# Kernel tuning notes

Measured on AMD Instinct MI355X. Metric: run time of the kernel, lower is better.

Reference implementation:

```python
import jax, jax.numpy as jnp
import numpy as np

B, S, D, H = 2, 2048, 1024, 16
DH = D // H  # head_dim = 64


def setup_inputs() -> dict:
    key = jax.random.key(0)
    ks = jax.random.split(key, 10)
    inp = {
        "query": jax.random.normal(ks[0], (B, S, D), jnp.float32),
        "key": jax.random.normal(ks[1], (B, S, D), jnp.float32),
        "value": jax.random.normal(ks[2], (B, S, D), jnp.float32),
        "mask": jnp.ones((B, S), jnp.int32),
        # per-head q/k/v projections stacked over the head axis [H, D, DH]
        "Wq": jax.random.normal(ks[3], (H, D, DH), jnp.float32) * 0.02,
        "bq": jnp.zeros((H, DH), jnp.float32),
        "Wk": jax.random.normal(ks[4], (H, D, DH), jnp.float32) * 0.02,
        "bk": jnp.zeros((H, DH), jnp.float32),
        "Wv": jax.random.normal(ks[5], (H, D, DH), jnp.float32) * 0.02,
        "bv": jnp.zeros((H, DH), jnp.float32),
        # output projection fc: Linear(D, D)
        "Wo": jax.random.normal(ks[6], (D, D), jnp.float32) * 0.02,
        "bo": jnp.zeros((D,), jnp.float32),
    }
    return inp


def reference(query, key, value, mask, Wq, bq, Wk, bk, Wv, bv, Wo, bo):
    scale = 1.0 / jnp.sqrt(jnp.asarray(DH, query.dtype))
    # batched per-head projections: [B,S,D] x [H,D,DH] -> [B,H,S,DH]
    q = jnp.einsum('bsd,hde->bhse', query, Wq) + bq[None, :, None, :]
    k = jnp.einsum('bsd,hde->bhse', key, Wk) + bk[None, :, None, :]
    v = jnp.einsum('bsd,hde->bhse', value, Wv) + bv[None, :, None, :]
    # scaled dot-product attention scores [B,H,Sq,Sk]
    scores = jnp.einsum('bhqe,bhke->bhqk', q, k) * scale
    scores = jnp.where(mask[:, None, None, :] == 0, jnp.asarray(-1e9, scores.dtype), scores)
    attn = jax.nn.softmax(scores, axis=-1)
    ctx = jnp.einsum('bhqk,bhke->bhqe', attn, v)          # [B,H,S,DH]
    ctx = ctx.transpose(0, 2, 1, 3).reshape(query.shape[0], -1, H * DH)  # concat heads
    return ctx @ Wo + bo
```

## Files before the change

### kernel.cpp

```cpp
#include <hip/hip_runtime.h>
#include <stdint.h>
#include <math.h>


typedef __attribute__((ext_vector_type(8))) short short8;
typedef __attribute__((ext_vector_type(4))) float floatx4;

#define LOG2E 1.44269504088896340736f

__device__ __forceinline__ unsigned short f32_bf16(float f) {
  union { float f; unsigned u; } c; c.f = f;
  return (unsigned short)((c.u + 0x7FFFu + ((c.u >> 16) & 1u)) >> 16);
}
__device__ __forceinline__ float bf16_f32(unsigned short u) {
  union { unsigned u; float f; } c; c.u = ((unsigned)u) << 16;
  return c.f;
}
__device__ __forceinline__ void gld16(const void* g, void* l) {
  __builtin_amdgcn_global_load_lds((const __attribute__((address_space(1))) void*)g,
                                   (__attribute__((address_space(3))) void*)l, 16, 0, 0);
}


__global__ __launch_bounds__(256) void prep_kernel(
    const float* __restrict__ qf, const float* __restrict__ kf, const float* __restrict__ vf,
    const float* __restrict__ w0, const float* __restrict__ w1, const float* __restrict__ w2,
    const float* __restrict__ wo, const int* __restrict__ mask,
    unsigned short* __restrict__ oq, unsigned short* __restrict__ ok, unsigned short* __restrict__ ov,
    unsigned short* __restrict__ o0, unsigned short* __restrict__ o1, unsigned short* __restrict__ o2,
    unsigned short* __restrict__ oo, float* __restrict__ mb) {
  __shared__ float t[32][33];
  const int y = blockIdx.y, bx = blockIdx.x;
  if (y < 3) {
    if (y == 0 && bx < 16) {
      int j = bx * 256 + threadIdx.x;
      mb[j] = (mask[j] == 0) ? (-1.0e9f * LOG2E) : 0.0f;
    }
    const float* in = (y == 0) ? qf : (y == 1) ? kf : vf;
    unsigned short* out = (y == 0) ? oq : (y == 1) ? ok : ov;
    int i = bx * 256 + threadIdx.x;
    float4 v = reinterpret_cast<const float4*>(in)[i];
    ushort4 o;
    o.x = f32_bf16(v.x); o.y = f32_bf16(v.y); o.z = f32_bf16(v.z); o.w = f32_bf16(v.w);
    reinterpret_cast<ushort4*>(out)[i] = o;
    return;
  }
  const int tx = threadIdx.x & 31, ty = threadIdx.x >> 5;
  const float* in; unsigned short* out; int R, C, z, r0, c0;
  if (bx < 3072) {
    const int zb = bx >> 6, rem = bx & 63;
    const int sel = zb >> 4; z = zb & 15;
    in = (sel == 0) ? w0 : (sel == 1) ? w1 : w2;
    out = (sel == 0) ? o0 : (sel == 1) ? o1 : o2;
    R = 1024; C = 64; r0 = (rem >> 1) * 32; c0 = (rem & 1) * 32;
  } else {
    const int t2 = bx - 3072;
    in = wo; out = oo; R = 1024; C = 1024; z = 0;
    r0 = (t2 >> 5) * 32; c0 = (t2 & 31) * 32;
  }
  const float* inp = in + (size_t)z * R * C;
  #pragma unroll
  for (int j = 0; j < 4; ++j)
    t[ty + j * 8][tx] = inp[(size_t)(r0 + ty + j * 8) * C + c0 + tx];
  __syncthreads();
  #pragma unroll
  for (int j = 0; j < 4; ++j)
    out[((size_t)z * C + c0 + ty + j * 8) * R + r0 + tx] = f32_bf16(t[tx][ty + j * 8]);
}


__global__ __launch_bounds__(512, 2) void gemm_proj_kernel(
    const unsigned short* __restrict__ qin, const unsigned short* __restrict__ kin,
    const unsigned short* __restrict__ vin,
    const unsigned short* __restrict__ WqT, const unsigned short* __restrict__ WkT,
    const unsigned short* __restrict__ WvT,
    const float* __restrict__ bq, const float* __restrict__ bk, const float* __restrict__ bv,
    unsigned short* __restrict__ Qp, unsigned short* __restrict__ Kp,
    unsigned short* __restrict__ Vt) {
  __shared__ unsigned short As[2][2][128 * 64];
  __shared__ unsigned short Bs[2][2][128 * 64];

  const int z = blockIdx.y;
  const int x = blockIdx.x;
  const int r = x & 7, q = x >> 3;
  int mt, nt;
  if (z < 2) { mt = r * 2 + (q >> 2); nt = q & 3; }
  else       { nt = r * 2 + (q >> 2); mt = q & 3; }
  const int blockM = mt * 256, blockN = nt * 256;

  const unsigned short* A  = (z == 0) ? qin : (z == 1) ? kin : WvT;
  const unsigned short* Bt = (z == 0) ? WqT : (z == 1) ? WkT : vin;
  const float* bias = (z == 0) ? bq : (z == 1) ? bk : bv;

  const int tid = threadIdx.x;
  const int w = tid >> 6, lane = tid & 63;
  const int quad = lane >> 4, l15 = lane & 15;
  const int wm = w & 1, wn = w >> 1;

  const int lr8 = lane >> 3;
  const int lc8 = lane & 7;
  const int gcs = lc8 ^ lr8;

  auto stage = [&](int k0, int buf) {
    #pragma unroll
    for (int h = 0; h < 2; ++h)
      #pragma unroll
      for (int s2 = 0; s2 < 2; ++s2) {
        const int rl = s2 * 64 + w * 8;
        gld16(A + (size_t)(blockM + h * 128 + rl + lr8) * 1024 + k0 + gcs * 8,
              &As[buf][h][rl * 64]);
      }
    #pragma unroll
    for (int h = 0; h < 2; ++h)
      #pragma unroll
      for (int s2 = 0; s2 < 2; ++s2) {
        const int rl = s2 * 64 + w * 8;
        gld16(Bt + (size_t)(blockN + h * 128 + rl + lr8) * 1024 + k0 + gcs * 8,
              &Bs[buf][h][rl * 64]);
      }
  };

  floatx4 acc[8][4];
  #pragma unroll
  for (int mi = 0; mi < 8; ++mi)
    #pragma unroll
    for (int ni = 0; ni < 4; ++ni)
      acc[mi][ni] = (floatx4){0.f, 0.f, 0.f, 0.f};

  stage(0, 0);
  __syncthreads();

  const int brb = (wn & 1) * 64;

  for (int st = 0; st < 16; ++st) {
    const int buf = st & 1;
    const unsigned short* Ah = &As[buf][wm][0];
    const unsigned short* Bh = &Bs[buf][wn >> 1][0];
    short8 af[4][2], b0[2][2], b1[2][2];

    if (st + 1 < 16) stage((st + 1) * 64, buf ^ 1);
    #pragma unroll
    for (int mi = 0; mi < 4; ++mi) {
      const int row = mi * 16 + l15;
      #pragma unroll
      for (int kk = 0; kk < 2; ++kk)
        af[mi][kk] = *(const short8*)(Ah + row * 64 + (((kk * 4 + quad) ^ (row & 7)) << 3));
    }
    #pragma unroll
    for (int ni = 0; ni < 2; ++ni) {
      const int row = brb + ni * 16 + l15;
      #pragma unroll
      for (int kk = 0; kk < 2; ++kk)
        b0[ni][kk] = *(const short8*)(Bh + row * 64 + (((kk * 4 + quad) ^ (row & 7)) << 3));
    }
    __builtin_amdgcn_s_barrier();
    __builtin_amdgcn_s_setprio(1);
    #pragma unroll
    for (int mi = 0; mi < 4; ++mi)
      #pragma unroll
      for (int ni = 0; ni < 2; ++ni)
        #pragma unroll
        for (int kk = 0; kk < 2; ++kk)
          acc[mi][ni] = __builtin_amdgcn_mfma_f32_16x16x32_bf16(af[mi][kk], b0[ni][kk], acc[mi][ni], 0, 0, 0);
    __builtin_amdgcn_s_setprio(0);
    __builtin_amdgcn_s_barrier();

    #pragma unroll
    for (int ni = 0; ni < 2; ++ni) {
      const int row = brb + (ni + 2) * 16 + l15;
      #pragma unroll
      for (int kk = 0; kk < 2; ++kk)
        b1[ni][kk] = *(const short8*)(Bh + row * 64 + (((kk * 4 + quad) ^ (row & 7)) << 3));
    }
    __builtin_amdgcn_s_barrier();
    __builtin_amdgcn_s_setprio(1);
    #pragma unroll
    for (int mi = 0; mi < 4; ++mi)
      #pragma unroll
      for (int ni = 0; ni < 2; ++ni)
        #pragma unroll
        for (int kk = 0; kk < 2; ++kk)
          acc[mi][ni + 2] = __builtin_amdgcn_mfma_f32_16x16x32_bf16(af[mi][kk], b1[ni][kk], acc[mi][ni + 2], 0, 0, 0);
    __builtin_amdgcn_s_setprio(0);
    __builtin_amdgcn_s_barrier();

    #pragma unroll
    for (int mi = 0; mi < 4; ++mi) {
      const int row = (mi + 4) * 16 + l15;
      #pragma unroll
      for (int kk = 0; kk < 2; ++kk)
        af[mi][kk] = *(const short8*)(Ah + row * 64 + (((kk * 4 + quad) ^ (row & 7)) << 3));
    }
    __builtin_amdgcn_s_barrier();
    __builtin_amdgcn_s_setprio(1);
    #pragma unroll
    for (int mi = 0; mi < 4; ++mi)
      #pragma unroll
      for (int ni = 0; ni < 2; ++ni)
        #pragma unroll
        for (int kk = 0; kk < 2; ++kk)
          acc[mi + 4][ni + 2] = __builtin_amdgcn_mfma_f32_16x16x32_bf16(af[mi][kk], b1[ni][kk], acc[mi + 4][ni + 2], 0, 0, 0);
    __builtin_amdgcn_s_setprio(0);
    __builtin_amdgcn_s_barrier();

    __builtin_amdgcn_s_setprio(1);
    #pragma unroll
    for (int mi = 0; mi < 4; ++mi)
      #pragma unroll
      for (int ni = 0; ni < 2; ++ni)
        #pragma unroll
        for (int kk = 0; kk < 2; ++kk)
          acc[mi + 4][ni] = __builtin_amdgcn_mfma_f32_16x16x32_bf16(af[mi][kk], b0[ni][kk], acc[mi + 4][ni], 0, 0, 0);
    __builtin_amdgcn_s_setprio(0);
    __syncthreads();
  }

  unsigned short* Cw = (w < 4) ? ((unsigned short*)As + w * 8192)
                               : ((unsigned short*)Bs + (w - 4) * 8192);
  const int pc = lc8 ^ lr8;

  if (z < 2) {
    unsigned short* outp = z ? Kp : Qp;
    const int n0 = blockN + wn * 64;
    const int m0 = blockM + wm * 128;
    float bn[4];
    #pragma unroll
    for (int ni = 0; ni < 4; ++ni) bn[ni] = bias[n0 + ni * 16 + l15];
    #pragma unroll
    for (int mi = 0; mi < 8; ++mi)
      #pragma unroll
      for (int ni = 0; ni < 4; ++ni)
        #pragma unroll
        for (int rr = 0; rr < 4; ++rr) {
          const int row = mi * 16 + quad * 4 + rr;
          const int col = ni * 16 + l15;
          Cw[row * 64 + (((col >> 3) ^ (row & 7)) << 3) + (col & 7)] =
              f32_bf16(acc[mi][ni][rr] + bn[ni]);
        }
    const size_t bb = (size_t)(m0 >> 11);
    const int h = n0 >> 6, s0 = m0 & 2047;
    unsigned short* dst = outp + ((bb * 16 + h) * 2048 + s0) * 64;
    #pragma unroll
    for (int ps = 0; ps < 16; ++ps) {
      const int lr = ps * 8 + lr8;
      *(short8*)(dst + lr * 64 + lc8 * 8) = *(const short8*)(Cw + lr * 64 + pc * 8);
    }
  } else {
    const int m0 = blockM + wm * 128;
    const int n0 = blockN + wn * 64;
    #pragma unroll
    for (int mi = 0; mi < 8; ++mi) {
      float bm[4];
      #pragma unroll
      for (int rr = 0; rr < 4; ++rr) bm[rr] = bias[m0 + mi * 16 + quad * 4 + rr];
      #pragma unroll
      for (int ni = 0; ni < 4; ++ni)
        #pragma unroll
        for (int rr = 0; rr < 4; ++rr) {
          const int row = mi * 16 + quad * 4 + rr;
          const int col = ni * 16 + l15;
          Cw[row * 64 + (((col >> 3) ^ (row & 7)) << 3) + (col & 7)] =
              f32_bf16(acc[mi][ni][rr] + bm[rr]);
        }
    }
    const size_t bb = (size_t)(n0 >> 11);
    const int s0 = n0 & 2047;
    unsigned short* dst = Vt + (bb * 1024 + m0) * 2048 + s0;
    #pragma unroll
    for (int ps = 0; ps < 16; ++ps) {
      const int lr = ps * 8 + lr8;
      *(short8*)(dst + (size_t)lr * 2048 + lc8 * 8) = *(const short8*)(Cw + lr * 64 + pc * 8);
    }
  }
}

__global__ __launch_bounds__(256) void gemm_out_kernel(
    const unsigned short* __restrict__ A, const unsigned short* __restrict__ Bt,
    const float* __restrict__ bias, float* __restrict__ out, int K, int N) {
  __shared__ unsigned short As[2][128 * 32];
  __shared__ unsigned short Bs[2][64 * 32];
  const int tid = threadIdx.x;
  const int w = tid >> 6, lane = tid & 63;
  const int quad = lane >> 4, l15 = lane & 15;
  const int wm = w & 1, wn = w >> 1;
  const int srow = lane >> 2;
  const int scol = (lane & 3) * 8;
  const int l = blockIdx.x, r = l & 7, j = l >> 3;
  const int blockM = (r * 4 + (j & 3)) * 128;
  const int blockN = (j >> 2) * 64;

  floatx4 acc[4][2];
  #pragma unroll
  for (int mi = 0; mi < 4; ++mi)
    #pragma unroll
    for (int ni = 0; ni < 2; ++ni)
      acc[mi][ni] = (floatx4){0.f, 0.f, 0.f, 0.f};

  const unsigned short* Arow = A + (size_t)blockM * K + (size_t)srow * K + scol;
  const unsigned short* Brow = Bt + (size_t)blockN * K + (size_t)srow * K + scol;

  auto stage = [&](int k0, int buf) {
    #pragma unroll
    for (int i = 0; i < 2; ++i) {
      int row = w * 32 + i * 16;
      gld16(Arow + (size_t)row * K + k0, As[buf] + row * 32);
    }
    gld16(Brow + (size_t)(w * 16) * K + k0, Bs[buf] + (w * 16) * 32);
  };

  const int iters = K >> 5;
  stage(0, 0);
  for (int it = 0; it < iters; ++it) {
    __syncthreads();
    if (it + 1 < iters) stage((it + 1) * 32, (it + 1) & 1);
    const unsigned short* Asb = As[it & 1];
    const unsigned short* Bsb = Bs[it & 1];
    short8 bf[2];
    #pragma unroll
    for (int ni = 0; ni < 2; ++ni)
      bf[ni] = *(const short8*)(Bsb + (wn * 32 + ni * 16 + l15) * 32 + quad * 8);
    #pragma unroll
    for (int mi = 0; mi < 4; ++mi) {
      short8 af = *(const short8*)(Asb + (wm * 64 + mi * 16 + l15) * 32 + quad * 8);
      #pragma unroll
      for (int ni = 0; ni < 2; ++ni)
        acc[mi][ni] = __builtin_amdgcn_mfma_f32_16x16x32_bf16(af, bf[ni], acc[mi][ni], 0, 0, 0);
    }
  }

  #pragma unroll
  for (int mi = 0; mi < 4; ++mi)
    #pragma unroll
    for (int ni = 0; ni < 2; ++ni) {
      const int n = blockN + wn * 32 + ni * 16 + l15;
      const float bv = bias[n];
      #pragma unroll
      for (int rr = 0; rr < 4; ++rr) {
        const int m = blockM + wm * 64 + mi * 16 + quad * 4 + rr;
        out[(size_t)m * N + n] = acc[mi][ni][rr] + bv;
      }
    }
}


__global__ __launch_bounds__(256) void attn_kernel(
    const unsigned short* __restrict__ Q, const unsigned short* __restrict__ Kg,
    const unsigned short* __restrict__ Vt, const float* __restrict__ maskAdd,
    unsigned short* __restrict__ ctx) {
  const int S = 2048;
  const int tid = threadIdx.x;
  const int w = tid >> 6, lane = tid & 63, quad = lane >> 4, l15 = lane & 15;
  const int l = blockIdx.x, r8 = l & 7, j8 = l >> 3;
  const int bh = r8 * 4 + (j8 & 3);
  const int qb = j8 >> 2;
  const int b = bh >> 4, h = bh & 15;
  const int q0 = qb * 128;

  __shared__ unsigned short Ks[2][128 * 64];
  __shared__ unsigned short Vs[2][64 * 128];
  __shared__ unsigned short Ps[4][32 * 64];
  unsigned short* Pw = Ps[w];

  const unsigned short* Qb = Q + (size_t)bh * S * 64;
  const unsigned short* Kb = Kg + (size_t)bh * S * 64;
  const unsigned short* Vb = Vt + (size_t)bh * 64 * S;
  const float* mb = maskAdd + (size_t)b * S;

  const float qs = 0.125f * LOG2E;
  short8 qf[2][2];
  #pragma unroll
  for (int mi = 0; mi < 2; ++mi)
    #pragma unroll
    for (int kq = 0; kq < 2; ++kq) {
      short8 v = *(const short8*)(Qb + (size_t)(q0 + w * 32 + mi * 16 + l15) * 64 + kq * 32 + quad * 8);
      #pragma unroll
      for (int jj = 0; jj < 8; ++jj)
        v[jj] = (short)f32_bf16(bf16_f32((unsigned short)v[jj]) * qs);
      qf[mi][kq] = v;
    }

  short8 onesf;
  #pragma unroll
  for (int jj = 0; jj < 8; ++jj) onesf[jj] = (short)0x3F80;

  floatx4 O[2][4], ls[2];
  #pragma unroll
  for (int mi = 0; mi < 2; ++mi) {
    #pragma unroll
    for (int ne = 0; ne < 4; ++ne) O[mi][ne] = (floatx4){0.f, 0.f, 0.f, 0.f};
    ls[mi] = (floatx4){0.f, 0.f, 0.f, 0.f};
  }

  auto stage_kv = [&](int t, int buf) {
    const int kv0 = t * 128;
    #pragma unroll
    for (int i = 0; i < 4; ++i) {
      int r0 = w * 32 + i * 8;
      int row = r0 + (lane >> 3);
      int cg = (lane & 7) ^ (row & 7);
      gld16(Kb + (size_t)(kv0 + row) * 64 + cg * 8, Ks[buf] + r0 * 64);
    }
    #pragma unroll
    for (int i = 0; i < 4; ++i) {
      int r0 = w * 16 + i * 4;
      int row = r0 + (lane >> 4);
      int p = lane & 15;
      int cg = (p & 8) | ((p & 7) ^ (row & 7));
      gld16(Vb + (size_t)row * S + kv0 + cg * 8, Vs[buf] + r0 * 128);
    }
  };

  stage_kv(0, 0);
  for (int t = 0; t < 16; ++t) {
    const int kv0 = t * 128;
    __syncthreads();
    float ma[8];
    #pragma unroll
    for (int ni = 0; ni < 8; ++ni) ma[ni] = mb[kv0 + ni * 16 + l15];
    if (t + 1 < 16) stage_kv(t + 1, (t + 1) & 1);
    const unsigned short* Ksb = Ks[t & 1];
    const unsigned short* Vsb = Vs[t & 1];

    #pragma unroll
    for (int ph = 0; ph < 2; ++ph) {
      floatx4 sc[2][4];
      #pragma unroll
      for (int ni = 0; ni < 4; ++ni) {
        const int key = (ph * 4 + ni) * 16 + l15;
        short8 kf0 = *(const short8*)(Ksb + key * 64 + ((quad) ^ (l15 & 7)) * 8);
        short8 kf1 = *(const short8*)(Ksb + key * 64 + ((4 + quad) ^ (l15 & 7)) * 8);
        #pragma unroll
        for (int mi = 0; mi < 2; ++mi) {
          floatx4 s = (floatx4){0.f, 0.f, 0.f, 0.f};
          s = __builtin_amdgcn_mfma_f32_16x16x32_bf16(qf[mi][0], kf0, s, 0, 0, 0);
          s = __builtin_amdgcn_mfma_f32_16x16x32_bf16(qf[mi][1], kf1, s, 0, 0, 0);
          sc[mi][ni] = s;
        }
      }
      #pragma unroll
      for (int mi = 0; mi < 2; ++mi)
        #pragma unroll
        for (int rr = 0; rr < 4; ++rr) {
          const int row = mi * 16 + quad * 4 + rr;
          const int g = (row + (row >> 3)) & 7;
          #pragma unroll
          for (int ni = 0; ni < 4; ++ni) {
            float p = __builtin_amdgcn_exp2f(sc[mi][ni][rr] + ma[ph * 4 + ni]);
            union { float f; unsigned u; } c; c.f = p;
            const int ch = (ni * 2 + (l15 >> 3)) ^ g;
            Pw[row * 64 + (ch & 7) * 8 + (l15 & 7)] = (unsigned short)(c.u >> 16);
          }
        }
      #pragma unroll
      for (int kkl = 0; kkl < 2; ++kkl) {
        const int kk = ph * 2 + kkl;
        short8 pfr[2], vfr[4];
        #pragma unroll
        for (int mi = 0; mi < 2; ++mi) {
          const int gp = (2 * mi + l15 + (l15 >> 3)) & 7;
          pfr[mi] = *(const short8*)(Pw + (mi * 16 + l15) * 64 + ((kkl * 4 + quad) ^ gp) * 8);
        }
        #pragma unroll
        for (int ne = 0; ne < 4; ++ne) {
          const int c = kk * 4 + quad;
          vfr[ne] = *(const short8*)(Vsb + (ne * 16 + l15) * 128 + ((c & 8) | ((c & 7) ^ (l15 & 7))) * 8);
        }
        #pragma unroll
        for (int mi = 0; mi < 2; ++mi) {
          #pragma unroll
          for (int ne = 0; ne < 4; ++ne)
            O[mi][ne] = __builtin_amdgcn_mfma_f32_16x16x32_bf16(pfr[mi], vfr[ne], O[mi][ne], 0, 0, 0);
          ls[mi] = __builtin_amdgcn_mfma_f32_16x16x32_bf16(pfr[mi], onesf, ls[mi], 0, 0, 0);
        }
      }
    }
  }

  #pragma unroll
  for (int mi = 0; mi < 2; ++mi)
    #pragma unroll
    for (int rr = 0; rr < 4; ++rr) {
      const float inv = __builtin_amdgcn_rcpf(ls[mi][rr]);
      const int s = q0 + w * 32 + mi * 16 + quad * 4 + rr;
      #pragma unroll
      for (int ne = 0; ne < 4; ++ne)
        ctx[((size_t)b * S + s) * 1024 + h * 64 + ne * 16 + l15] = f32_bf16(O[mi][ne][rr] * inv);
    }
}


extern "C" void kernel_launch(void* const* d_in, const int* in_sizes, int n_in,
                              void* d_out, int out_size, void* d_ws, size_t ws_size,
                              hipStream_t stream) {
  const float* query = (const float*)d_in[0];
  const float* key   = (const float*)d_in[1];
  const float* value = (const float*)d_in[2];
  const int*   mask  = (const int*)d_in[3];
  const float* Wq = (const float*)d_in[4];
  const float* bq = (const float*)d_in[5];
  const float* Wk = (const float*)d_in[6];
  const float* bk = (const float*)d_in[7];
  const float* Wv = (const float*)d_in[8];
  const float* bv = (const float*)d_in[9];
  const float* Wo = (const float*)d_in[10];
  const float* bo = (const float*)d_in[11];
  float* out = (float*)d_out;

  char* ws = (char*)d_ws;
  const size_t MB = 1024 * 1024;
  unsigned short* qin  = (unsigned short*)(ws + 0);
  unsigned short* kin  = (unsigned short*)(ws + 8 * MB);
  unsigned short* vin  = (unsigned short*)(ws + 16 * MB);
  unsigned short* WqT  = (unsigned short*)(ws + 24 * MB);
  unsigned short* WkT  = (unsigned short*)(ws + 26 * MB);
  unsigned short* WvT  = (unsigned short*)(ws + 28 * MB);
  unsigned short* WoT  = (unsigned short*)(ws + 30 * MB);
  unsigned short* Qp   = (unsigned short*)(ws + 32 * MB);
  unsigned short* Kp   = (unsigned short*)(ws + 40 * MB);
  unsigned short* Vt   = (unsigned short*)(ws + 48 * MB);
  float* maskAdd       = (float*)(ws + 56 * MB);
  unsigned short* ctxb = qin;

  prep_kernel<<<dim3(4096, 4), 256, 0, stream>>>(query, key, value, Wq, Wk, Wv, Wo, mask,
                                                 qin, kin, vin, WqT, WkT, WvT, WoT, maskAdd);
  gemm_proj_kernel<<<dim3(64, 3), 512, 0, stream>>>(qin, kin, vin, WqT, WkT, WvT,
                                                    bq, bk, bv, Qp, Kp, Vt);
  attn_kernel<<<dim3(512), 256, 0, stream>>>(Qp, Kp, Vt, maskAdd, ctxb);
  gemm_out_kernel<<<dim3(512), 256, 0, stream>>>(ctxb, WoT, bo, out, 1024, 1024);
}
```

Baseline: 231.0 us.

## Transpose score MFMA, vectorize P stores, sum softmax denominators in registers, widen out-GEMM K tile

In the attention kernel the QK^T MFMA now has its operands swapped, so each lane holds four consecutive keys for one query row. The exponentials are packed into 4-wide bf16 stores to LDS, the mask is loaded as a float4, and the row sum is accumulated in registers and reduced with shuffles at the end instead of using an extra ones-vector MFMA. The output GEMM stages 64-wide K tiles with an XOR swizzle, which halves the loop iterations and barriers. The changes are meant to cut MFMA count, scalar LDS stores and bank conflicts, at the cost of more registers and some shuffle work.

```diff
diff --git a/kernel.cpp b/kernel.cpp
--- a/kernel.cpp
+++ b/kernel.cpp
@@ -4,6 +4,7 @@
 
 
 typedef __attribute__((ext_vector_type(8))) short short8;
+typedef __attribute__((ext_vector_type(4))) short short4v;
 typedef __attribute__((ext_vector_type(4))) float floatx4;
 
 #define LOG2E 1.44269504088896340736f
@@ -274,17 +275,18 @@
   }
 }
 
+
 __global__ __launch_bounds__(256) void gemm_out_kernel(
     const unsigned short* __restrict__ A, const unsigned short* __restrict__ Bt,
     const float* __restrict__ bias, float* __restrict__ out, int K, int N) {
-  __shared__ unsigned short As[2][128 * 32];
-  __shared__ unsigned short Bs[2][64 * 32];
+  __shared__ unsigned short As[2][128 * 64];
+  __shared__ unsigned short Bs[2][64 * 64];
   const int tid = threadIdx.x;
   const int w = tid >> 6, lane = tid & 63;
   const int quad = lane >> 4, l15 = lane & 15;
   const int wm = w & 1, wn = w >> 1;
-  const int srow = lane >> 2;
-  const int scol = (lane & 3) * 8;
+  const int lr8 = lane >> 3, lc8 = lane & 7;
+  const int gcs = lc8 ^ lr8;
   const int l = blockIdx.x, r = l & 7, j = l >> 3;
   const int blockM = (r * 4 + (j & 3)) * 128;
   const int blockN = (j >> 2) * 64;
@@ -296,35 +298,44 @@
     for (int ni = 0; ni < 2; ++ni)
       acc[mi][ni] = (floatx4){0.f, 0.f, 0.f, 0.f};
 
-  const unsigned short* Arow = A + (size_t)blockM * K + (size_t)srow * K + scol;
-  const unsigned short* Brow = Bt + (size_t)blockN * K + (size_t)srow * K + scol;
-
   auto stage = [&](int k0, int buf) {
     #pragma unroll
+    for (int i = 0; i < 4; ++i) {
+      const int rl = w * 32 + i * 8;
+      gld16(A + (size_t)(blockM + rl + lr8) * K + k0 + gcs * 8, As[buf] + rl * 64);
+    }
+    #pragma unroll
     for (int i = 0; i < 2; ++i) {
-      int row = w * 32 + i * 16;
-      gld16(Arow + (size_t)row * K + k0, As[buf] + row * 32);
-    }
-    gld16(Brow + (size_t)(w * 16) * K + k0, Bs[buf] + (w * 16) * 32);
+      const int rl = w * 16 + i * 8;
+      gld16(Bt + (size_t)(blockN + rl + lr8) * K + k0 + gcs * 8, Bs[buf] + rl * 64);
+    }
   };
 
-  const int iters = K >> 5;
+  const int iters = K >> 6;
   stage(0, 0);
   for (int it = 0; it < iters; ++it) {
     __syncthreads();
-    if (it + 1 < iters) stage((it + 1) * 32, (it + 1) & 1);
+    if (it + 1 < iters) stage((it + 1) * 64, (it + 1) & 1);
     const unsigned short* Asb = As[it & 1];
     const unsigned short* Bsb = Bs[it & 1];
-    short8 bf[2];
-    #pragma unroll
-    for (int ni = 0; ni < 2; ++ni)
-      bf[ni] = *(const short8*)(Bsb + (wn * 32 + ni * 16 + l15) * 32 + quad * 8);
+    short8 bf[2][2];
+    #pragma unroll
+    for (int ni = 0; ni < 2; ++ni) {
+      const int row = wn * 32 + ni * 16 + l15;
+      #pragma unroll
+      for (int kk = 0; kk < 2; ++kk)
+        bf[ni][kk] = *(const short8*)(Bsb + row * 64 + (((kk * 4 + quad) ^ (row & 7)) << 3));
+    }
     #pragma unroll
     for (int mi = 0; mi < 4; ++mi) {
-      short8 af = *(const short8*)(Asb + (wm * 64 + mi * 16 + l15) * 32 + quad * 8);
-      #pragma unroll
-      for (int ni = 0; ni < 2; ++ni)
-        acc[mi][ni] = __builtin_amdgcn_mfma_f32_16x16x32_bf16(af, bf[ni], acc[mi][ni], 0, 0, 0);
+      const int row = wm * 64 + mi * 16 + l15;
+      #pragma unroll
+      for (int kk = 0; kk < 2; ++kk) {
+        short8 af = *(const short8*)(Asb + row * 64 + (((kk * 4 + quad) ^ (row & 7)) << 3));
+        #pragma unroll
+        for (int ni = 0; ni < 2; ++ni)
+          acc[mi][ni] = __builtin_amdgcn_mfma_f32_16x16x32_bf16(af, bf[ni][kk], acc[mi][ni], 0, 0, 0);
+      }
     }
   }
 
@@ -379,17 +390,12 @@
       qf[mi][kq] = v;
     }
 
-  short8 onesf;
-  #pragma unroll
-  for (int jj = 0; jj < 8; ++jj) onesf[jj] = (short)0x3F80;
-
-  floatx4 O[2][4], ls[2];
-  #pragma unroll
-  for (int mi = 0; mi < 2; ++mi) {
+  floatx4 O[2][4];
+  float lsum[2] = {0.f, 0.f};
+  #pragma unroll
+  for (int mi = 0; mi < 2; ++mi)
     #pragma unroll
     for (int ne = 0; ne < 4; ++ne) O[mi][ne] = (floatx4){0.f, 0.f, 0.f, 0.f};
-    ls[mi] = (floatx4){0.f, 0.f, 0.f, 0.f};
-  }
 
   auto stage_kv = [&](int t, int buf) {
     const int kv0 = t * 128;
@@ -414,78 +420,74 @@
   for (int t = 0; t < 16; ++t) {
     const int kv0 = t * 128;
     __syncthreads();
-    float ma[8];
-    #pragma unroll
-    for (int ni = 0; ni < 8; ++ni) ma[ni] = mb[kv0 + ni * 16 + l15];
     if (t + 1 < 16) stage_kv(t + 1, (t + 1) & 1);
     const unsigned short* Ksb = Ks[t & 1];
     const unsigned short* Vsb = Vs[t & 1];
 
     #pragma unroll
     for (int ph = 0; ph < 2; ++ph) {
-      floatx4 sc[2][4];
       #pragma unroll
       for (int ni = 0; ni < 4; ++ni) {
-        const int key = (ph * 4 + ni) * 16 + l15;
-        short8 kf0 = *(const short8*)(Ksb + key * 64 + ((quad) ^ (l15 & 7)) * 8);
-        short8 kf1 = *(const short8*)(Ksb + key * 64 + ((4 + quad) ^ (l15 & 7)) * 8);
+        const int key16 = (ph * 4 + ni) * 16;
+        short8 kf0 = *(const short8*)(Ksb + (key16 + l15) * 64 + ((quad ^ (l15 & 7)) * 8));
+        short8 kf1 = *(const short8*)(Ksb + (key16 + l15) * 64 + (((4 + quad) ^ (l15 & 7)) * 8));
+        const floatx4 m4 = *(const floatx4*)(mb + kv0 + key16 + quad * 4);
         #pragma unroll
         for (int mi = 0; mi < 2; ++mi) {
           floatx4 s = (floatx4){0.f, 0.f, 0.f, 0.f};
-          s = __builtin_amdgcn_mfma_f32_16x16x32_bf16(qf[mi][0], kf0, s, 0, 0, 0);
-          s = __builtin_amdgcn_mfma_f32_16x16x32_bf16(qf[mi][1], kf1, s, 0, 0, 0);
-          sc[mi][ni] = s;
+          s = __builtin_amdgcn_mfma_f32_16x16x32_bf16(kf0, qf[mi][0], s, 0, 0, 0);
+          s = __builtin_amdgcn_mfma_f32_16x16x32_bf16(kf1, qf[mi][1], s, 0, 0, 0);
+          short4v pk;
+          #pragma unroll
+          for (int rr = 0; rr < 4; ++rr) {
+            const float p = __builtin_amdgcn_exp2f(s[rr] + m4[rr]);
+            const unsigned short pb = f32_bf16(p);
+            pk[rr] = (short)pb;
+            lsum[mi] += bf16_f32(pb);
+          }
+          const int row = mi * 16 + l15;
+          const int phys = (ni * 2 + (quad >> 1)) ^ (l15 & 7);
+          *(short4v*)(Pw + row * 64 + phys * 8 + (quad & 1) * 4) = pk;
         }
       }
-      #pragma unroll
-      for (int mi = 0; mi < 2; ++mi)
-        #pragma unroll
-        for (int rr = 0; rr < 4; ++rr) {
-          const int row = mi * 16 + quad * 4 + rr;
-          const int g = (row + (row >> 3)) & 7;
-          #pragma unroll
-          for (int ni = 0; ni < 4; ++ni) {
-            float p = __builtin_amdgcn_exp2f(sc[mi][ni][rr] + ma[ph * 4 + ni]);
-            union { float f; unsigned u; } c; c.f = p;
-            const int ch = (ni * 2 + (l15 >> 3)) ^ g;
-            Pw[row * 64 + (ch & 7) * 8 + (l15 & 7)] = (unsigned short)(c.u >> 16);
-          }
-        }
+      asm volatile("" ::: "memory");
       #pragma unroll
       for (int kkl = 0; kkl < 2; ++kkl) {
         const int kk = ph * 2 + kkl;
         short8 pfr[2], vfr[4];
         #pragma unroll
-        for (int mi = 0; mi < 2; ++mi) {
-          const int gp = (2 * mi + l15 + (l15 >> 3)) & 7;
-          pfr[mi] = *(const short8*)(Pw + (mi * 16 + l15) * 64 + ((kkl * 4 + quad) ^ gp) * 8);
-        }
+        for (int mi = 0; mi < 2; ++mi)
+          pfr[mi] = *(const short8*)(Pw + (mi * 16 + l15) * 64 + (((kkl * 4 + quad) ^ (l15 & 7)) << 3));
         #pragma unroll
         for (int ne = 0; ne < 4; ++ne) {
           const int c = kk * 4 + quad;
           vfr[ne] = *(const short8*)(Vsb + (ne * 16 + l15) * 128 + ((c & 8) | ((c & 7) ^ (l15 & 7))) * 8);
         }
         #pragma unroll
-        for (int mi = 0; mi < 2; ++mi) {
+        for (int mi = 0; mi < 2; ++mi)
           #pragma unroll
           for (int ne = 0; ne < 4; ++ne)
             O[mi][ne] = __builtin_amdgcn_mfma_f32_16x16x32_bf16(pfr[mi], vfr[ne], O[mi][ne], 0, 0, 0);
-          ls[mi] = __builtin_amdgcn_mfma_f32_16x16x32_bf16(pfr[mi], onesf, ls[mi], 0, 0, 0);
-        }
       }
-    }
-  }
-
-  #pragma unroll
-  for (int mi = 0; mi < 2; ++mi)
+      asm volatile("" ::: "memory");
+    }
+  }
+
+  #pragma unroll
+  for (int mi = 0; mi < 2; ++mi) {
+    float v = lsum[mi];
+    v += __shfl_xor(v, 16);
+    v += __shfl_xor(v, 32);
     #pragma unroll
     for (int rr = 0; rr < 4; ++rr) {
-      const float inv = __builtin_amdgcn_rcpf(ls[mi][rr]);
+      const float lv = __shfl(v, quad * 4 + rr);
+      const float inv = __builtin_amdgcn_rcpf(lv);
       const int s = q0 + w * 32 + mi * 16 + quad * 4 + rr;
       #pragma unroll
       for (int ne = 0; ne < 4; ++ne)
         ctx[((size_t)b * S + s) * 1024 + h * 64 + ne * 16 + l15] = f32_bf16(O[mi][ne][rr] * inv);
     }
+  }
 }
 
 
```

Result: slower. 238.0 us (+3.1%).
